# Kernel tuning notes

Measured on AMD Instinct MI355X. Metric: run time of the kernel, lower is better.

The kernel has to match this reference:

```python
import jax, jax.numpy as jnp
import numpy as np

B, C, H, W = 4, 192, 256, 256
P = 8          # patch_size; d_model = P, input_size = P*P
R = 4          # FFN expansion ratio
SLOPE = 0.01   # torch default leaky_relu negative_slope


def _conv(x, w, pad):
    return jax.lax.conv_general_dilated(x, w, (1, 1), pad,
                                        dimension_numbers=('NCHW', 'OIHW', 'NCHW'))


def setup_inputs() -> dict:
    key = jax.random.key(0)
    ks = jax.random.split(key, 16)
    p2 = P * P
    s = 0.05
    return {
        'x':  jax.random.normal(ks[0], (B, C, H, W), jnp.float32),
        # per-window linear attention params (torch Linear stored as (in,out))
        'Wq': jax.random.normal(ks[1], (p2, P), jnp.float32) * s,
        'bq': jnp.zeros((P,), jnp.float32),
        'Wk': jax.random.normal(ks[2], (p2, P), jnp.float32) * s,
        'bk': jnp.zeros((P,), jnp.float32),
        'Wv': jax.random.normal(ks[3], (p2, P), jnp.float32) * s,
        'bv': jnp.zeros((P,), jnp.float32),
        'Wo': jax.random.normal(ks[4], (P, p2), jnp.float32) * s,
        'bo': jnp.zeros((p2,), jnp.float32),
        # FFN conv params
        'W1': jax.random.normal(ks[5], (C * R, C, 1, 1), jnp.float32) * s,
        'b1': jnp.zeros((C * R,), jnp.float32),
        'W2': jax.random.normal(ks[6], (C * R, C * R, 3, 3), jnp.float32) * s,
        'b2': jnp.zeros((C * R,), jnp.float32),
        'W3': jax.random.normal(ks[7], (C, C * R, 1, 1), jnp.float32) * s,
        'b3': jnp.zeros((C,), jnp.float32),
    }


def reference(x, Wq, bq, Wk, bk, Wv, bv, Wo, bo, W1, b1, W2, b2, W3, b3):
    Bb, Cc, Hh, Ww = x.shape
    nh, nw = Hh // P, Ww // P
    N = nh * nw
    # crop patches: (B, N, C, P*P), window-major row order (i over rows, j over cols)
    xp = (x.reshape(Bb, Cc, nh, P, nw, P)
           .transpose(0, 2, 4, 1, 3, 5)
           .reshape(Bb, N, Cc, P * P))
    # softplus-kernel linear attention over the CHANNEL axis (weight is CxC per window)
    q = jax.nn.softplus(xp @ Wq + bq)            # (B,N,C,P)
    k = jax.nn.softplus(xp @ Wk + bk)            # (B,N,C,P)
    v = xp @ Wv + bv                              # (B,N,C,P)
    w = jnp.einsum('bncd,bnhd->bnch', q, k)      # (B,N,C,C)
    r = jnp.einsum('bnch,bnhd->bncd', w, v)      # (B,N,C,P)
    attn = r @ Wo + bo                            # (B,N,C,P*P)
    y = xp + attn                                 # in-place residual in the original
    # Merge_patches: cat along height then reshape == contiguous reinterpret
    feat = (y.reshape(Bb, N, Cc, P, P)
             .transpose(0, 2, 1, 3, 4)
             .reshape(Bb, Cc, nh * P, nw * P))
    h = jax.nn.leaky_relu(_conv(feat, W1, 'VALID') + b1[:, None, None], SLOPE)
    h = jax.nn.leaky_relu(_conv(h, W2, 'SAME') + b2[:, None, None], SLOPE)
    out = jax.nn.leaky_relu(_conv(h, W3, 'VALID') + b3[:, None, None], SLOPE)
    return out
```

## Files before the change

### kernel.cpp

```cpp
#include <hip/hip_runtime.h>
#include <stdint.h>
#include <math.h>

typedef _Float16 half_t;
typedef _Float16 f16x8 __attribute__((ext_vector_type(8)));
typedef float f32x4 __attribute__((ext_vector_type(4)));

#define SLOPE 0.01f

__device__ inline float leaky(float v) { return v > 0.f ? v : SLOPE * v; }

__device__ inline void stage16(const half_t* g, half_t* l) {
    __builtin_amdgcn_global_load_lds(
        (const __attribute__((address_space(1))) unsigned int*)g,
        (__attribute__((address_space(3))) unsigned int*)l, 16, 0, 0);
}

__device__ inline float softplusf(float v) {
    return v > 20.f ? v : log1pf(expf(v));
}

__global__ void prep_kernel(const float* __restrict__ W1, const float* __restrict__ W2,
                            const float* __restrict__ W3,
                            half_t* __restrict__ B1w, half_t* __restrict__ B2w,
                            half_t* __restrict__ B3w)
{
    const unsigned idx = blockIdx.x * 256u + threadIdx.x;
    const unsigned n2 = 768u * 6912u;
    if (idx < n2) {
        unsigned oc = idx / 6912u;
        unsigned rem = idx - oc * 6912u;
        unsigned tap = rem / 768u;
        unsigned ic = rem - tap * 768u;
        unsigned ky = tap / 3u, kx = tap - ky * 3u;
        B2w[idx] = (half_t)W2[(((size_t)oc * 768u + ic) * 3u + ky) * 3u + kx];
    } else if (idx < n2 + 147456u) {
        unsigned i = idx - n2;
        B1w[i] = (half_t)W1[i];
    } else if (idx < n2 + 294912u) {
        unsigned i = idx - n2 - 147456u;
        B3w[i] = (half_t)W3[i];
    }
}

__global__ __launch_bounds__(256, 2)
void attn_kernel(const float* __restrict__ x,
                 const float* __restrict__ Wq, const float* __restrict__ bq,
                 const float* __restrict__ Wk, const float* __restrict__ bk,
                 const float* __restrict__ Wv, const float* __restrict__ bv,
                 const float* __restrict__ Wo, const float* __restrict__ bo,
                 half_t* __restrict__ featN)
{
    __shared__ half_t xls[192 * 65];
    __shared__ float wqL[512], wkL[512], wvL[512], woL[512];
    __shared__ float bqL[8], bkL[8], bvL[8], boL[64];
    __shared__ float kls[192 * 9], vls[192 * 9];
    __shared__ float sls[64];

    const int t = threadIdx.x;
    const int blk = blockIdx.x;
    const int b = blk >> 10;
    const int n = blk & 1023;
    const int wi = n >> 5, wj = n & 31;

    for (int i = t; i < 512; i += 256) {
        wqL[i] = Wq[i]; wkL[i] = Wk[i]; wvL[i] = Wv[i]; woL[i] = Wo[i];
    }
    if (t < 8)  { bqL[t] = bq[t]; bkL[t] = bk[t]; bvL[t] = bv[t]; }
    if (t < 64) boL[t] = bo[t];

    #pragma unroll
    for (int i = 0; i < 6; ++i) {
        int idx = t + i * 256;
        int c = idx >> 3, py = idx & 7;
        const float* src = x + (((size_t)b * 192 + c) * 256 + (wi * 8 + py)) * 256 + wj * 8;
        float4 v0 = *(const float4*)src;
        float4 v1 = *(const float4*)(src + 4);
        half_t* dst = &xls[c * 65 + py * 8];
        dst[0] = (half_t)v0.x; dst[1] = (half_t)v0.y; dst[2] = (half_t)v0.z; dst[3] = (half_t)v0.w;
        dst[4] = (half_t)v1.x; dst[5] = (half_t)v1.y; dst[6] = (half_t)v1.z; dst[7] = (half_t)v1.w;
    }
    __syncthreads();

    float qf[8], kf[8], vf[8];
    if (t < 192) {
        #pragma unroll
        for (int d = 0; d < 8; ++d) { qf[d] = bqL[d]; kf[d] = bkL[d]; vf[d] = bvL[d]; }
        const half_t* xr = &xls[t * 65];
        for (int p = 0; p < 64; ++p) {
            float xv = (float)xr[p];
            const float* wqp = &wqL[p * 8];
            const float* wkp = &wkL[p * 8];
            const float* wvp = &wvL[p * 8];
            #pragma unroll
            for (int d = 0; d < 8; ++d) {
                qf[d] += xv * wqp[d];
                kf[d] += xv * wkp[d];
                vf[d] += xv * wvp[d];
            }
        }
        #pragma unroll
        for (int d = 0; d < 8; ++d) {
            qf[d] = softplusf(qf[d]);
            kf[d] = softplusf(kf[d]);
            kls[t * 9 + d] = kf[d];
            vls[t * 9 + d] = vf[d];
        }
    }
    __syncthreads();
    if (t < 64) {
        int e = t >> 3, dd = t & 7;
        float s = 0.f;
        for (int c = 0; c < 192; ++c) s += kls[c * 9 + e] * vls[c * 9 + dd];
        sls[t] = s;
    }
    __syncthreads();
    if (t < 192) {
        float rf[8];
        #pragma unroll
        for (int d = 0; d < 8; ++d) {
            float s = 0.f;
            #pragma unroll
            for (int e = 0; e < 8; ++e) s += qf[e] * sls[e * 8 + d];
            rf[d] = s;
        }
        half_t* xr = &xls[t * 65];
        for (int p = 0; p < 64; ++p) {
            float a = boL[p];
            #pragma unroll
            for (int d = 0; d < 8; ++d) a += rf[d] * woL[d * 64 + p];
            xr[p] = (half_t)((float)xr[p] + a);
        }
    }
    __syncthreads();
    half_t* dst = featN + ((size_t)b * 65536 + (size_t)n * 64) * 192;
    for (int i = 0; i < 48; ++i) {
        int idx = t + i * 256;
        int p = idx / 192, c = idx - p * 192;
        dst[idx] = xls[c * 65 + p];
    }
}

__global__ __launch_bounds__(256, 2)
void conv1_kernel(const half_t* __restrict__ featN, const half_t* __restrict__ B1w,
                  const float* __restrict__ b1, half_t* __restrict__ h1p, int batch)
{
    __shared__ half_t As[128 * 64];
    __shared__ half_t Bs[128 * 64];
    const int t = threadIdx.x;
    const int lane = t & 63;
    const int w = t >> 6;
    const int m0 = blockIdx.x * 128;
    const int n0 = blockIdx.y * 128;
    const int wm = (w >> 1) * 64, wn = (w & 1) * 64;
    const int rbase = t >> 3;
    const int g = (t & 7) ^ (rbase & 7);
    const int ar = lane & 15, kc = lane >> 4;

    f32x4 acc[4][4];
    #pragma unroll
    for (int i = 0; i < 4; ++i)
        #pragma unroll
        for (int j = 0; j < 4; ++j) acc[i][j] = (f32x4){0.f, 0.f, 0.f, 0.f};

    const size_t mb = (size_t)batch * 65536 + m0;

    for (int s = 0; s < 3; ++s) {
        const int k0 = s * 64;
        const half_t* ga = featN + (mb + rbase) * 192 + k0 + g * 8;
        const half_t* gb = B1w + (size_t)(n0 + rbase) * 192 + k0 + g * 8;
        half_t* la = As + t * 8;
        half_t* lb = Bs + t * 8;
        #pragma unroll
        for (int i = 0; i < 4; ++i) {
            stage16(ga + (size_t)32 * i * 192, la + 2048 * i);
            stage16(gb + (size_t)32 * i * 192, lb + 2048 * i);
        }
        __syncthreads();
        #pragma unroll
        for (int kh = 0; kh < 2; ++kh) {
            f16x8 af[4], bfr[4];
            const int c = kh * 4 + kc;
            #pragma unroll
            for (int mf = 0; mf < 4; ++mf) {
                int r = wm + mf * 16 + ar;
                af[mf] = *(const f16x8*)&As[(r * 8 + (c ^ (r & 7))) * 8];
            }
            #pragma unroll
            for (int nf = 0; nf < 4; ++nf) {
                int r = wn + nf * 16 + ar;
                bfr[nf] = *(const f16x8*)&Bs[(r * 8 + (c ^ (r & 7))) * 8];
            }
            #pragma unroll
            for (int mf = 0; mf < 4; ++mf)
                #pragma unroll
                for (int nf = 0; nf < 4; ++nf)
                    acc[mf][nf] = __builtin_amdgcn_mfma_f32_16x16x32_f16(af[mf], bfr[nf], acc[mf][nf], 0, 0, 0);
        }
        __syncthreads();
    }

    const int y = m0 >> 8, x0 = m0 & 255;
    half_t* outrow = h1p + ((size_t)(y + 1) * 258 + (x0 + 1)) * 768;
    #pragma unroll
    for (int nf = 0; nf < 4; ++nf) {
        int n = n0 + wn + nf * 16 + ar;
        float bias = b1[n];
        #pragma unroll
        for (int mf = 0; mf < 4; ++mf) {
            #pragma unroll
            for (int r4 = 0; r4 < 4; ++r4) {
                int local = wm + mf * 16 + kc * 4 + r4;
                outrow[(size_t)local * 768 + n] = (half_t)leaky(acc[mf][nf][r4] + bias);
            }
        }
    }
}

__device__ __forceinline__ void c2_stage_A(half_t* As, int buf, int h,
    const half_t* __restrict__ h1p, int y, int kstep, int t, int cg)
{
    const int tap = kstep / 12, icc = kstep - tap * 12;
    const int ky = tap / 3, kx = tap - ky * 3;
    const int row0 = t >> 3;
    const half_t* g = h1p + ((size_t)(y + ky) * 258 + (kx + h * 128 + row0)) * 768
                      + icc * 64 + cg;
    half_t* l = As + (buf * 2 + h) * 8192 + t * 8;
    stage16(g, l);
    stage16(g + (size_t)64 * 768, l + 4096);
}

__device__ __forceinline__ void c2_stage_B(half_t* Bs, int buf, int h,
    const half_t* __restrict__ B2w, int n0, int kstep, int t, int cg)
{
    const int tap = kstep / 12, icc = kstep - tap * 12;
    const int row0 = t >> 3;
    const half_t* g = B2w + (size_t)(n0 + h * 128 + row0) * 6912
                      + tap * 768 + icc * 64 + cg;
    half_t* l = Bs + (buf * 2 + h) * 8192 + t * 8;
    stage16(g, l);
    stage16(g + (size_t)64 * 6912, l + 4096);
}

#define C2_PHASE(MQ, NQ, BUF, RD_A, RD_B, STAGE_CODE, VMCNT_CODE)                   \
  {                                                                                  \
    if (RD_A) {                                                                      \
      _Pragma("unroll")                                                              \
      for (int mf = 0; mf < 4; ++mf) {                                               \
        _Pragma("unroll")                                                            \
        for (int kh = 0; kh < 2; ++kh) {                                             \
          int lr = wm * 64 + mf * 16 + ar;                                           \
          int ch = (kh * 4 + kc) ^ (lr & 7);                                         \
          af[mf][kh] = *(const f16x8*)&As[((BUF) * 2 + (MQ)) * 8192 + lr * 64 + ch * 8]; \
        }                                                                            \
      }                                                                              \
    }                                                                                \
    if (RD_B) {                                                                      \
      _Pragma("unroll")                                                              \
      for (int nf = 0; nf < 2; ++nf) {                                               \
        _Pragma("unroll")                                                            \
        for (int kh = 0; kh < 2; ++kh) {                                             \
          int lc = wn * 32 + nf * 16 + ar;                                           \
          int ch = (kh * 4 + kc) ^ (lc & 7);                                         \
          bf[nf][kh] = *(const f16x8*)&Bs[((BUF) * 2 + (NQ)) * 8192 + lc * 64 + ch * 8]; \
        }                                                                            \
      }                                                                              \
    }                                                                                \
    STAGE_CODE                                                                       \
    VMCNT_CODE                                                                       \
    __builtin_amdgcn_s_barrier();                                                    \
    asm volatile("s_waitcnt lgkmcnt(0)" ::: "memory");                               \
    __builtin_amdgcn_sched_barrier(0);                                               \
    __builtin_amdgcn_s_setprio(1);                                                   \
    _Pragma("unroll")                                                                \
    for (int kh = 0; kh < 2; ++kh)                                                   \
      _Pragma("unroll")                                                              \
      for (int mf = 0; mf < 4; ++mf)                                                 \
        _Pragma("unroll")                                                            \
        for (int nf = 0; nf < 2; ++nf)                                               \
          acc[(MQ) * 2 + (NQ)][mf][nf] = __builtin_amdgcn_mfma_f32_16x16x32_f16(     \
              af[mf][kh], bf[nf][kh], acc[(MQ) * 2 + (NQ)][mf][nf], 0, 0, 0);        \
    __builtin_amdgcn_s_setprio(0);                                                   \
    __builtin_amdgcn_s_barrier();                                                    \
  }

#define C2_VM4 { asm volatile("s_waitcnt vmcnt(4)" ::: "memory"); }
#define C2_VM0 { asm volatile("s_waitcnt vmcnt(0)" ::: "memory"); }
#define C2_NOP { }

__global__ __launch_bounds__(512, 2)
void conv2_kernel(const half_t* __restrict__ h1p, const half_t* __restrict__ B2w,
                  const float* __restrict__ b2, half_t* __restrict__ h2)
{
    __shared__ half_t As[4 * 8192];
    __shared__ half_t Bs[4 * 8192];

    const int t = threadIdx.x;
    const int lane = t & 63;
    const int w = t >> 6;
    const int wm = w >> 2, wn = w & 3;
    const int ar = lane & 15, kc = lane >> 4;
    const int cg = (((t & 7) ^ ((t >> 3) & 7)) << 3);

    const int bid = blockIdx.x;
    const int xcd = bid & 7, sid = bid >> 3;
    const int wg = xcd * 96 + sid;
    const int mtile = wg / 3;
    const int nt = wg - mtile * 3;
    const int y = mtile;
    const int m0 = mtile * 256;
    const int n0 = nt * 256;

    f32x4 acc[4][4][2];
    #pragma unroll
    for (int q = 0; q < 4; ++q)
        #pragma unroll
        for (int i = 0; i < 4; ++i)
            #pragma unroll
            for (int j = 0; j < 2; ++j) acc[q][i][j] = (f32x4){0.f, 0.f, 0.f, 0.f};

    f16x8 af[4][2], bf[2][2];

    c2_stage_A(As, 0, 0, h1p, y, 0, t, cg);
    c2_stage_A(As, 0, 1, h1p, y, 0, t, cg);
    c2_stage_B(Bs, 0, 0, B2w, n0, 0, t, cg);
    c2_stage_B(Bs, 0, 1, B2w, n0, 0, t, cg);
    c2_stage_A(As, 1, 0, h1p, y, 1, t, cg);
    c2_stage_B(Bs, 1, 1, B2w, n0, 1, t, cg);
    asm volatile("s_waitcnt vmcnt(0)" ::: "memory");
    __builtin_amdgcn_s_barrier();

    for (int i = 0; i < 53; ++i) {
        const int k1 = 2 * i + 1;
        const int k2 = 2 * i + 2;
        C2_PHASE(0, 0, 0, 1, 1,
                 { c2_stage_A(As, 1, 1, h1p, y, k1, t, cg);
                   c2_stage_B(Bs, 1, 0, B2w, n0, k1, t, cg); }, C2_NOP)
        C2_PHASE(0, 1, 0, 0, 1, C2_NOP, C2_NOP)
        C2_PHASE(1, 1, 0, 1, 0,
                 { c2_stage_A(As, 0, 0, h1p, y, k2, t, cg); }, C2_NOP)
        C2_PHASE(1, 0, 0, 0, 1,
                 { c2_stage_B(Bs, 0, 1, B2w, n0, k2, t, cg); }, C2_VM4)
        C2_PHASE(0, 0, 1, 1, 1,
                 { c2_stage_A(As, 0, 1, h1p, y, k2, t, cg);
                   c2_stage_B(Bs, 0, 0, B2w, n0, k2, t, cg); }, C2_NOP)
        C2_PHASE(0, 1, 1, 0, 1, C2_NOP, C2_NOP)
        C2_PHASE(1, 1, 1, 1, 0,
                 { c2_stage_A(As, 1, 0, h1p, y, k1 + 2, t, cg); }, C2_NOP)
        C2_PHASE(1, 0, 1, 0, 1,
                 { c2_stage_B(Bs, 1, 1, B2w, n0, k1 + 2, t, cg); }, C2_VM4)
    }
    C2_PHASE(0, 0, 0, 1, 1,
             { c2_stage_A(As, 1, 1, h1p, y, 107, t, cg);
               c2_stage_B(Bs, 1, 0, B2w, n0, 107, t, cg); }, C2_NOP)
    C2_PHASE(0, 1, 0, 0, 1, C2_NOP, C2_NOP)
    C2_PHASE(1, 1, 0, 1, 0, C2_NOP, C2_NOP)
    C2_PHASE(1, 0, 0, 0, 1, C2_NOP, C2_VM0)
    C2_PHASE(0, 0, 1, 1, 1, C2_NOP, C2_NOP)
    C2_PHASE(0, 1, 1, 0, 1, C2_NOP, C2_NOP)
    C2_PHASE(1, 1, 1, 1, 0, C2_NOP, C2_NOP)
    C2_PHASE(1, 0, 1, 0, 1, C2_NOP, C2_NOP)

    #pragma unroll
    for (int q = 0; q < 4; ++q) {
        const int mq = q >> 1, nq = q & 1;
        #pragma unroll
        for (int nf = 0; nf < 2; ++nf) {
            const int col = n0 + nq * 128 + wn * 32 + nf * 16 + ar;
            const float bias = b2[col];
            #pragma unroll
            for (int mf = 0; mf < 4; ++mf) {
                const int row = m0 + mq * 128 + wm * 64 + mf * 16 + kc * 4;
                half_t* op = h2 + (size_t)row * 768 + col;
                #pragma unroll
                for (int r4 = 0; r4 < 4; ++r4)
                    op[(size_t)r4 * 768] = (half_t)leaky(acc[q][mf][nf][r4] + bias);
            }
        }
    }
}

__global__ __launch_bounds__(256, 2)
void conv3_kernel(const half_t* __restrict__ h2, const half_t* __restrict__ B3w,
                  const float* __restrict__ b3, float* __restrict__ out, int batch)
{
    __shared__ half_t As[128 * 64];
    __shared__ half_t Bs[192 * 64];
    const int t = threadIdx.x;
    const int lane = t & 63;
    const int w = t >> 6;
    const int m0 = blockIdx.x * 128;
    const int wm = (w >> 1) * 64;
    const int wn = (w & 1) * 96;
    const int rbase = t >> 3;
    const int g = (t & 7) ^ (rbase & 7);
    const int ar = lane & 15, kc = lane >> 4;

    f32x4 acc[4][6];
    #pragma unroll
    for (int i = 0; i < 4; ++i)
        #pragma unroll
        for (int j = 0; j < 6; ++j) acc[i][j] = (f32x4){0.f, 0.f, 0.f, 0.f};

    for (int s = 0; s < 12; ++s) {
        const int k0 = s * 64;
        const half_t* ga = h2 + (size_t)(m0 + rbase) * 768 + k0 + g * 8;
        const half_t* gb = B3w + (size_t)rbase * 768 + k0 + g * 8;
        half_t* la = As + t * 8;
        half_t* lb = Bs + t * 8;
        #pragma unroll
        for (int i = 0; i < 4; ++i) stage16(ga + (size_t)32 * i * 768, la + 2048 * i);
        #pragma unroll
        for (int i = 0; i < 6; ++i) stage16(gb + (size_t)32 * i * 768, lb + 2048 * i);
        __syncthreads();
        #pragma unroll
        for (int kh = 0; kh < 2; ++kh) {
            f16x8 af[4], bfr[6];
            const int c = kh * 4 + kc;
            #pragma unroll
            for (int mf = 0; mf < 4; ++mf) {
                int r = wm + mf * 16 + ar;
                af[mf] = *(const f16x8*)&As[(r * 8 + (c ^ (r & 7))) * 8];
            }
            #pragma unroll
            for (int nf = 0; nf < 6; ++nf) {
                int r = wn + nf * 16 + ar;
                bfr[nf] = *(const f16x8*)&Bs[(r * 8 + (c ^ (r & 7))) * 8];
            }
            #pragma unroll
            for (int mf = 0; mf < 4; ++mf)
                #pragma unroll
                for (int nf = 0; nf < 6; ++nf)
                    acc[mf][nf] = __builtin_amdgcn_mfma_f32_16x16x32_f16(af[mf], bfr[nf], acc[mf][nf], 0, 0, 0);
        }
        __syncthreads();
    }

    #pragma unroll
    for (int nf = 0; nf < 6; ++nf) {
        int n = wn + nf * 16 + ar;
        float bias = b3[n];
        float* op = out + ((size_t)batch * 192 + n) * 65536 + m0;
        #pragma unroll
        for (int mf = 0; mf < 4; ++mf) {
            int local = wm + mf * 16 + kc * 4;
            f32x4 v;
            #pragma unroll
            for (int r4 = 0; r4 < 4; ++r4) v[r4] = leaky(acc[mf][nf][r4] + bias);
            *(f32x4*)(op + local) = v;
        }
    }
}

extern "C" void kernel_launch(void* const* d_in, const int* in_sizes, int n_in,
                              void* d_out, int out_size, void* d_ws, size_t ws_size,
                              hipStream_t stream)
{
    const float* x  = (const float*)d_in[0];
    const float* Wq = (const float*)d_in[1];
    const float* bq = (const float*)d_in[2];
    const float* Wk = (const float*)d_in[3];
    const float* bk = (const float*)d_in[4];
    const float* Wv = (const float*)d_in[5];
    const float* bv = (const float*)d_in[6];
    const float* Wo = (const float*)d_in[7];
    const float* bo = (const float*)d_in[8];
    const float* W1 = (const float*)d_in[9];
    const float* b1 = (const float*)d_in[10];
    const float* W2 = (const float*)d_in[11];
    const float* b2 = (const float*)d_in[12];
    const float* W3 = (const float*)d_in[13];
    const float* b3 = (const float*)d_in[14];

    char* ws = (char*)d_ws;
    const size_t OFF_B1   = 0;
    const size_t OFF_B3   = 294912;
    const size_t OFF_B2   = 589824;
    const size_t OFF_FEAT = 11206656;
    const size_t OFF_H1P  = 111869952;
    const size_t OFF_H2   = 214124544;
    const size_t WS_NEED  = 314787840;
    if (ws_size < WS_NEED) return;

    half_t* B1w   = (half_t*)(ws + OFF_B1);
    half_t* B3w   = (half_t*)(ws + OFF_B3);
    half_t* B2w   = (half_t*)(ws + OFF_B2);
    half_t* featN = (half_t*)(ws + OFF_FEAT);
    half_t* h1p   = (half_t*)(ws + OFF_H1P);
    half_t* h2    = (half_t*)(ws + OFF_H2);

    hipMemsetAsync(h1p, 0, 102254592, stream);
    prep_kernel<<<21888, 256, 0, stream>>>(W1, W2, W3, B1w, B2w, B3w);
    attn_kernel<<<4096, 256, 0, stream>>>(x, Wq, bq, Wk, bk, Wv, bv, Wo, bo, featN);

    for (int b = 0; b < 4; ++b) {
        conv1_kernel<<<dim3(512, 6), 256, 0, stream>>>(featN, B1w, b1, h1p, b);
        conv2_kernel<<<768, 512, 0, stream>>>(h1p, B2w, b2, h2);
        conv3_kernel<<<dim3(512, 1), 256, 0, stream>>>(h2, B3w, b3, (float*)d_out, b);
    }
}
```

Baseline: 3.151 ms.

## Restructure conv2 MFMA loop with register-double-buffered fragments and finer waitcnts

The conv2 GEMM main loop is rescheduled so that A and B fragments for both M/N quadrants are held in registers (af/bf get an extra quadrant dimension). LDS reads for the next quadrant are issued ahead of the MFMA block, and partial lgkmcnt waits replace the full wait-then-barrier pattern in every phase. Global-to-LDS staging is also regrouped so each half-buffer is staged once its last reader has finished. The aim is to overlap LDS reads with MFMA work and cut barrier and wait stalls, at the cost of more VGPRs, which risks spilling or lower occupancy under launch_bounds(512,2).

```diff
diff --git a/kernel.cpp b/kernel.cpp
--- a/kernel.cpp
+++ b/kernel.cpp
@@ -242,51 +242,44 @@
     stage16(g + (size_t)64 * 6912, l + 4096);
 }
 
-#define C2_PHASE(MQ, NQ, BUF, RD_A, RD_B, STAGE_CODE, VMCNT_CODE)                   \
-  {                                                                                  \
-    if (RD_A) {                                                                      \
-      _Pragma("unroll")                                                              \
-      for (int mf = 0; mf < 4; ++mf) {                                               \
-        _Pragma("unroll")                                                            \
-        for (int kh = 0; kh < 2; ++kh) {                                             \
-          int lr = wm * 64 + mf * 16 + ar;                                           \
-          int ch = (kh * 4 + kc) ^ (lr & 7);                                         \
-          af[mf][kh] = *(const f16x8*)&As[((BUF) * 2 + (MQ)) * 8192 + lr * 64 + ch * 8]; \
-        }                                                                            \
-      }                                                                              \
-    }                                                                                \
-    if (RD_B) {                                                                      \
-      _Pragma("unroll")                                                              \
-      for (int nf = 0; nf < 2; ++nf) {                                               \
-        _Pragma("unroll")                                                            \
-        for (int kh = 0; kh < 2; ++kh) {                                             \
-          int lc = wn * 32 + nf * 16 + ar;                                           \
-          int ch = (kh * 4 + kc) ^ (lc & 7);                                         \
-          bf[nf][kh] = *(const f16x8*)&Bs[((BUF) * 2 + (NQ)) * 8192 + lc * 64 + ch * 8]; \
-        }                                                                            \
-      }                                                                              \
-    }                                                                                \
-    STAGE_CODE                                                                       \
-    VMCNT_CODE                                                                       \
-    __builtin_amdgcn_s_barrier();                                                    \
-    asm volatile("s_waitcnt lgkmcnt(0)" ::: "memory");                               \
-    __builtin_amdgcn_sched_barrier(0);                                               \
-    __builtin_amdgcn_s_setprio(1);                                                   \
-    _Pragma("unroll")                                                                \
-    for (int kh = 0; kh < 2; ++kh)                                                   \
-      _Pragma("unroll")                                                              \
-      for (int mf = 0; mf < 4; ++mf)                                                 \
-        _Pragma("unroll")                                                            \
-        for (int nf = 0; nf < 2; ++nf)                                               \
-          acc[(MQ) * 2 + (NQ)][mf][nf] = __builtin_amdgcn_mfma_f32_16x16x32_f16(     \
-              af[mf][kh], bf[nf][kh], acc[(MQ) * 2 + (NQ)][mf][nf], 0, 0, 0);        \
-    __builtin_amdgcn_s_setprio(0);                                                   \
-    __builtin_amdgcn_s_barrier();                                                    \
+#define SBAR __builtin_amdgcn_s_barrier()
+#define SB0  __builtin_amdgcn_sched_barrier(0)
+#define LGKM(N) asm volatile("s_waitcnt lgkmcnt(" #N ")" ::: "memory")
+#define VMC(N)  asm volatile("s_waitcnt vmcnt(" #N ")" ::: "memory")
+
+#define RDA(MQ, BUF)                                                             \
+  _Pragma("unroll")                                                              \
+  for (int mf = 0; mf < 4; ++mf)                                                 \
+    _Pragma("unroll")                                                            \
+    for (int kh = 0; kh < 2; ++kh) {                                             \
+      const int lr = wm * 64 + mf * 16 + ar;                                     \
+      const int ch = (kh * 4 + kc) ^ (lr & 7);                                   \
+      af[MQ][mf][kh] = *(const f16x8*)&As[((BUF)*2 + (MQ))*8192 + lr*64 + ch*8]; \
+    }
+
+#define RDB(NQ, BUF)                                                             \
+  _Pragma("unroll")                                                              \
+  for (int nf = 0; nf < 2; ++nf)                                                 \
+    _Pragma("unroll")                                                            \
+    for (int kh = 0; kh < 2; ++kh) {                                             \
+      const int lc = wn * 32 + nf * 16 + ar;                                     \
+      const int ch = (kh * 4 + kc) ^ (lc & 7);                                   \
+      bf[NQ][nf][kh] = *(const f16x8*)&Bs[((BUF)*2 + (NQ))*8192 + lc*64 + ch*8]; \
+    }
+
+#define MMA16(MQ, NQ)                                                            \
+  {                                                                              \
+    __builtin_amdgcn_s_setprio(1);                                               \
+    _Pragma("unroll")                                                            \
+    for (int kh = 0; kh < 2; ++kh)                                               \
+      _Pragma("unroll")                                                          \
+      for (int mf = 0; mf < 4; ++mf)                                             \
+        _Pragma("unroll")                                                        \
+        for (int nf = 0; nf < 2; ++nf)                                           \
+          acc[(MQ)*2+(NQ)][mf][nf] = __builtin_amdgcn_mfma_f32_16x16x32_f16(     \
+              af[MQ][mf][kh], bf[NQ][nf][kh], acc[(MQ)*2+(NQ)][mf][nf], 0, 0, 0);\
+    __builtin_amdgcn_s_setprio(0);                                               \
   }
-
-#define C2_VM4 { asm volatile("s_waitcnt vmcnt(4)" ::: "memory"); }
-#define C2_VM0 { asm volatile("s_waitcnt vmcnt(0)" ::: "memory"); }
-#define C2_NOP { }
 
 __global__ __launch_bounds__(512, 2)
 void conv2_kernel(const half_t* __restrict__ h1p, const half_t* __restrict__ B2w,
@@ -319,47 +312,102 @@
             #pragma unroll
             for (int j = 0; j < 2; ++j) acc[q][i][j] = (f32x4){0.f, 0.f, 0.f, 0.f};
 
-    f16x8 af[4][2], bf[2][2];
+    f16x8 af[2][4][2];
+    f16x8 bf[2][2][2];
 
     c2_stage_A(As, 0, 0, h1p, y, 0, t, cg);
     c2_stage_A(As, 0, 1, h1p, y, 0, t, cg);
     c2_stage_B(Bs, 0, 0, B2w, n0, 0, t, cg);
     c2_stage_B(Bs, 0, 1, B2w, n0, 0, t, cg);
     c2_stage_A(As, 1, 0, h1p, y, 1, t, cg);
+    c2_stage_A(As, 1, 1, h1p, y, 1, t, cg);
+    c2_stage_B(Bs, 1, 0, B2w, n0, 1, t, cg);
     c2_stage_B(Bs, 1, 1, B2w, n0, 1, t, cg);
-    asm volatile("s_waitcnt vmcnt(0)" ::: "memory");
-    __builtin_amdgcn_s_barrier();
+    VMC(0);
+    SBAR; SB0;
+    RDB(0, 0); SB0;
+    RDA(0, 0);
 
     for (int i = 0; i < 53; ++i) {
-        const int k1 = 2 * i + 1;
         const int k2 = 2 * i + 2;
-        C2_PHASE(0, 0, 0, 1, 1,
-                 { c2_stage_A(As, 1, 1, h1p, y, k1, t, cg);
-                   c2_stage_B(Bs, 1, 0, B2w, n0, k1, t, cg); }, C2_NOP)
-        C2_PHASE(0, 1, 0, 0, 1, C2_NOP, C2_NOP)
-        C2_PHASE(1, 1, 0, 1, 0,
-                 { c2_stage_A(As, 0, 0, h1p, y, k2, t, cg); }, C2_NOP)
-        C2_PHASE(1, 0, 0, 0, 1,
-                 { c2_stage_B(Bs, 0, 1, B2w, n0, k2, t, cg); }, C2_VM4)
-        C2_PHASE(0, 0, 1, 1, 1,
-                 { c2_stage_A(As, 0, 1, h1p, y, k2, t, cg);
-                   c2_stage_B(Bs, 0, 0, B2w, n0, k2, t, cg); }, C2_NOP)
-        C2_PHASE(0, 1, 1, 0, 1, C2_NOP, C2_NOP)
-        C2_PHASE(1, 1, 1, 1, 0,
-                 { c2_stage_A(As, 1, 0, h1p, y, k1 + 2, t, cg); }, C2_NOP)
-        C2_PHASE(1, 0, 1, 0, 1,
-                 { c2_stage_B(Bs, 1, 1, B2w, n0, k1 + 2, t, cg); }, C2_VM4)
-    }
-    C2_PHASE(0, 0, 0, 1, 1,
-             { c2_stage_A(As, 1, 1, h1p, y, 107, t, cg);
-               c2_stage_B(Bs, 1, 0, B2w, n0, 107, t, cg); }, C2_NOP)
-    C2_PHASE(0, 1, 0, 0, 1, C2_NOP, C2_NOP)
-    C2_PHASE(1, 1, 0, 1, 0, C2_NOP, C2_NOP)
-    C2_PHASE(1, 0, 0, 0, 1, C2_NOP, C2_VM0)
-    C2_PHASE(0, 0, 1, 1, 1, C2_NOP, C2_NOP)
-    C2_PHASE(0, 1, 1, 0, 1, C2_NOP, C2_NOP)
-    C2_PHASE(1, 1, 1, 1, 0, C2_NOP, C2_NOP)
-    C2_PHASE(1, 0, 1, 0, 1, C2_NOP, C2_NOP)
+        const int k3 = 2 * i + 3;
+        RDB(1, 0); SB0;
+        RDA(1, 0);
+        LGKM(12); SB0;
+        MMA16(0, 0);
+        SBAR;
+        c2_stage_A(As, 0, 0, h1p, y, k2, t, cg);
+        c2_stage_B(Bs, 0, 0, B2w, n0, k2, t, cg);
+        LGKM(8); SB0;
+        MMA16(0, 1);
+        SBAR;
+        LGKM(0); SB0;
+        MMA16(1, 1);
+        SBAR;
+        c2_stage_A(As, 0, 1, h1p, y, k2, t, cg);
+        c2_stage_B(Bs, 0, 1, B2w, n0, k2, t, cg);
+        VMC(8);
+        SBAR; SB0;
+        MMA16(1, 0);
+        SB0;
+        RDB(0, 1); SB0;
+        RDA(0, 1);
+        SBAR;
+        RDB(1, 1); SB0;
+        RDA(1, 1);
+        LGKM(12); SB0;
+        MMA16(0, 0);
+        SBAR;
+        c2_stage_A(As, 1, 0, h1p, y, k3, t, cg);
+        c2_stage_B(Bs, 1, 0, B2w, n0, k3, t, cg);
+        LGKM(8); SB0;
+        MMA16(0, 1);
+        SBAR;
+        LGKM(0); SB0;
+        MMA16(1, 1);
+        SBAR;
+        c2_stage_A(As, 1, 1, h1p, y, k3, t, cg);
+        c2_stage_B(Bs, 1, 1, B2w, n0, k3, t, cg);
+        VMC(8);
+        SBAR; SB0;
+        MMA16(1, 0);
+        SB0;
+        RDB(0, 0); SB0;
+        RDA(0, 0);
+        SBAR;
+    }
+    {
+        RDB(1, 0); SB0;
+        RDA(1, 0);
+        LGKM(12); SB0;
+        MMA16(0, 0);
+        SBAR;
+        LGKM(8); SB0;
+        MMA16(0, 1);
+        SBAR;
+        LGKM(0); SB0;
+        MMA16(1, 1);
+        SBAR;
+        VMC(0);
+        SBAR; SB0;
+        MMA16(1, 0);
+        SB0;
+        RDB(0, 1); SB0;
+        RDA(0, 1);
+        SBAR;
+        RDB(1, 1); SB0;
+        RDA(1, 1);
+        LGKM(12); SB0;
+        MMA16(0, 0);
+        SBAR;
+        LGKM(8); SB0;
+        MMA16(0, 1);
+        SBAR;
+        LGKM(0); SB0;
+        MMA16(1, 1);
+        SBAR;
+        MMA16(1, 0);
+    }
 
     #pragma unroll
     for (int q = 0; q < 4; ++q) {
```

Result: faster. 2.907 ms (-7.7%).
